# Kernel tuning notes

Measured on AMD Instinct MI355X. Metric: run time of the kernel, lower is better.

## Reference

```python
import jax, jax.numpy as jnp
import numpy as np

K = 10
BN_EPS = 1e-5


def _edgeconv(x, W, b, gamma, beta):
    """DGCNN EdgeConv: kNN on x, edge feat [x_i, x_j - x_i], Linear->(BN)->ReLU, max over k.
    x: [N, C]; W: [2C, Cout]; gamma/beta: [Cout] or None."""
    sq = jnp.sum(x * x, axis=1)                      # [N]
    dist = sq[:, None] + sq[None, :] - 2.0 * (x @ x.T)  # [N, N] squared dists
    _, idx = jax.lax.top_k(-dist, K)                 # [N, K] (includes self)
    xj = x[idx]                                      # [N, K, C] gather
    xi = jnp.broadcast_to(x[:, None, :], xj.shape)   # [N, K, C]
    e = jnp.concatenate([xi, xj - xi], axis=-1)      # [N, K, 2C]
    h = e @ W + b                                    # [N, K, Cout]
    if gamma is not None:                            # BatchNorm1d (training-mode batch stats)
        mu = h.mean(axis=(0, 1))
        var = h.var(axis=(0, 1))
        h = (h - mu) * jax.lax.rsqrt(var + BN_EPS) * gamma + beta
    h = jax.nn.relu(h)
    return h.max(axis=1)                             # [N, Cout]


def _aggregate(f, seg_ids, num_segments):
    return jax.ops.segment_max(f, seg_ids, num_segments=num_segments)


def setup_inputs() -> dict:
    key = jax.random.key(0)
    ks = jax.random.split(key, 12)
    N, B = 16384, 64
    x = jax.random.normal(ks[0], (N, 3), dtype=jnp.float32)
    n_pts = jnp.full((B,), N // B, dtype=jnp.int32)

    def lin(k, fi, fo):
        s = 1.0 / np.sqrt(fi)
        kw, kb = jax.random.split(k)
        return (jax.random.uniform(kw, (fi, fo), jnp.float32, -s, s),
                jax.random.uniform(kb, (fo,), jnp.float32, -s, s))

    W1, b1 = lin(ks[1], 6, 64)
    W2, b2 = lin(ks[2], 128, 64)
    W3, b3 = lin(ks[3], 128, 64)
    W4, b4 = lin(ks[4], 128, 64)
    Wp, bp = lin(ks[5], 256, 128)
    g1 = jnp.ones((64,), jnp.float32); be1 = jnp.zeros((64,), jnp.float32)
    g3 = jnp.ones((64,), jnp.float32); be3 = jnp.zeros((64,), jnp.float32)
    return {"x": x, "n_pts": n_pts,
            "W1": W1, "b1": b1, "g1": g1, "be1": be1,
            "W2": W2, "b2": b2,
            "W3": W3, "b3": b3, "g3": g3, "be3": be3,
            "W4": W4, "b4": b4,
            "Wp": Wp, "bp": bp}


def reference(x, n_pts, W1, b1, g1, be1, W2, b2, W3, b3, g3, be3, W4, b4, Wp, bp):
    N = x.shape[0]
    B = n_pts.shape[0]
    seg_ids = jnp.repeat(jnp.arange(B, dtype=jnp.int32), n_pts, total_repeat_length=N)

    f1 = _edgeconv(x,  W1, b1, g1,  be1)   # [N, 64]
    f2 = _edgeconv(f1, W2, b2, None, None)
    f3 = _edgeconv(f2, W3, b3, g3,  be3)
    f4 = _edgeconv(f3, W4, b4, None, None)

    p = jnp.concatenate([_aggregate(f, seg_ids, B) for f in (f1, f2, f3, f4)], axis=1)  # [B, 256]
    f = jnp.tanh(p @ Wp + bp)              # [B, 128]
    f = f / (jnp.linalg.norm(f, axis=1, keepdims=True) + 1e-9)
    return f
```

## Files before the change

### kernel.cpp

```cpp
#include <hip/hip_runtime.h>
#include <hip/hip_bf16.h>

constexpr int N = 16384;
constexpr int KNN = 10;
constexpr int CF = 64;
constexpr int NS64 = 12;
constexpr int NS3 = 12;

#define FBIG 1e30f

typedef __attribute__((ext_vector_type(8))) __bf16 bfv8;
typedef __attribute__((ext_vector_type(4))) float f32x4;

#define TOPK_INSERT(dval, jval)                                            \
  if ((dval) < bmax) {                                                     \
    float mv = bd[0]; int slot = 0;                                        \
    _Pragma("unroll") for (int s_ = 1; s_ < 10; ++s_)                      \
      if (bd[s_] > mv) { mv = bd[s_]; slot = s_; }                         \
    _Pragma("unroll") for (int s_ = 0; s_ < 10; ++s_)                      \
      if (slot == s_) { bd[s_] = (dval); bi[s_] = (jval); }                \
    bmax = bd[0];                                                          \
    _Pragma("unroll") for (int s_ = 1; s_ < 10; ++s_)                      \
      bmax = fmaxf(bmax, bd[s_]);                                          \
  }

__device__ inline ushort bf16_rne(float x) {
  unsigned u = __float_as_uint(x);
  return (ushort)((u + 0x7FFFu + ((u >> 16) & 1u)) >> 16);
}
__device__ inline float bf16_to_f(ushort h) { return __uint_as_float(((unsigned)h) << 16); }

__global__ __launch_bounds__(256) void pack3_kernel(const float* __restrict__ X,
                                                    float4* __restrict__ xp,
                                                    int* __restrict__ gtauI,
                                                    float* __restrict__ accum) {
  int i = blockIdx.x * 256 + threadIdx.x;
  float x0 = X[3 * i], x1 = X[3 * i + 1], x2 = X[3 * i + 2];
  float s = fmaf(x0, x0, fmaf(x1, x1, x2 * x2));
  xp[i] = make_float4(x0, x1, x2, s);
  gtauI[i] = 0x7F7F7F7F;
  if (blockIdx.x == 0 && threadIdx.x < 128) accum[threadIdx.x] = 0.f;
}

__global__ __launch_bounds__(256) void prep128s_kernel(const float* __restrict__ X,
                                                       ushort* __restrict__ Xp,
                                                       float* __restrict__ sq,
                                                       int* __restrict__ gtauI,
                                                       float* __restrict__ accum) {
  int i = blockIdx.x * 256 + threadIdx.x;
  int n = i >> 4, k4 = (i & 15) << 2;
  float4 v = ((const float4*)X)[i];
  float vv[4] = {v.x, v.y, v.z, v.w};
  ushort h[4], lo[4];
#pragma unroll
  for (int k = 0; k < 4; ++k) {
    h[k] = bf16_rne(vv[k]);
    lo[k] = bf16_rne(vv[k] - bf16_to_f(h[k]));
  }
  ushort* row = Xp + (size_t)n * 128;
  *(ushort4*)(row + k4) = make_ushort4(h[0], h[1], h[2], h[3]);
  *(ushort4*)(row + 64 + k4) = make_ushort4(lo[0], lo[1], lo[2], lo[3]);
  float ps = fmaf(vv[0], vv[0], fmaf(vv[1], vv[1], fmaf(vv[2], vv[2], vv[3] * vv[3])));
#pragma unroll
  for (int m = 1; m < 16; m <<= 1) ps += __shfl_xor(ps, m, 16);
  if ((threadIdx.x & 15) == 0) {
    sq[n] = ps;
    gtauI[n] = 0x7F7F7F7F;
  }
  if (blockIdx.x == 0 && threadIdx.x < 128) accum[threadIdx.x] = 0.f;
}

__global__ __launch_bounds__(256, 3) void knn64w_kernel(const ushort* __restrict__ Xp,
                                                        const float* __restrict__ sq,
                                                        int* __restrict__ gtauI,
                                                        float* __restrict__ dpart,
                                                        ushort* __restrict__ ipart) {
  __shared__ float bufD[4][64 * 33];
  __shared__ ushort bufI[4][64 * 34];
  __shared__ __align__(16) float tauS[4][64];
  __shared__ int cntS[4][64];

  const int tid = threadIdx.x;
  const int w = tid >> 6, l = tid & 63, lp = l & 15, g = l >> 4;
  const int rg = blockIdx.x / NS64, cs = blockIdx.x % NS64;
  const int wbase = rg * 256 + w * 64;
  const int myrow = wbase + l;
  const int c0 = (512 * cs) / NS64, c1 = (512 * (cs + 1)) / NS64;

  tauS[w][l] = FBIG;
  cntS[w][l] = 0;
  __builtin_amdgcn_wave_barrier();

  bfv8 aH1[4], aH2[4], aL1[4], aL2[4];
#pragma unroll
  for (int rt = 0; rt < 4; ++rt) {
    const size_t ao = (size_t)(wbase + rt * 16 + lp) * 128 + g * 8;
    aH1[rt] = *(const bfv8*)&Xp[ao];
    aH2[rt] = *(const bfv8*)&Xp[ao + 32];
    aL1[rt] = *(const bfv8*)&Xp[ao + 64];
    aL2[rt] = *(const bfv8*)&Xp[ao + 96];
  }
  float sqi[16];
#pragma unroll
  for (int rt = 0; rt < 4; ++rt)
#pragma unroll
    for (int r = 0; r < 4; ++r) sqi[rt * 4 + r] = sq[wbase + rt * 16 + g * 4 + r];

  float bd[10]; int bi[10]; float bmax = FBIG; float lastPub = FBIG;
#pragma unroll
  for (int s = 0; s < 10; ++s) { bd[s] = FBIG; bi[s] = 0x7fffffff; }
  int gt = 0x7F7F7F7F;

  for (int t = c0; t < c1; ++t) {
    const int col0 = t * 32 + lp;
    const int col1 = col0 + 16;
    const size_t bo0 = (size_t)col0 * 128 + g * 8;
    bfv8 p0 = *(const bfv8*)&Xp[bo0];
    bfv8 p1 = *(const bfv8*)&Xp[bo0 + 32];
    bfv8 p2 = *(const bfv8*)&Xp[bo0 + 64];
    bfv8 p3 = *(const bfv8*)&Xp[bo0 + 96];
    const size_t bo1 = (size_t)col1 * 128 + g * 8;
    bfv8 q0 = *(const bfv8*)&Xp[bo1];
    bfv8 q1 = *(const bfv8*)&Xp[bo1 + 32];
    bfv8 q2 = *(const bfv8*)&Xp[bo1 + 64];
    bfv8 q3 = *(const bfv8*)&Xp[bo1 + 96];
    float sj0 = sq[col0];
    float sj1 = sq[col1];
    int gtn = gtauI[myrow];

    __builtin_amdgcn_wave_barrier();
    {
      const int c = cntS[w][l];
      if (c) {
        const float* bD = &bufD[w][l * 33];
        const ushort* bI = &bufI[w][l * 34];
#pragma unroll 1
        for (int j = 0; j < c; ++j) {
          float d = bD[j];
          int ii = (int)bI[j];
          TOPK_INSERT(d, ii);
        }
        cntS[w][l] = 0;
      }
      tauS[w][l] = fminf(bmax, __int_as_float(gt));
      if (bmax < lastPub) {
        atomicMin(&gtauI[myrow], __float_as_int(bmax));
        lastPub = bmax;
      }
    }
    __builtin_amdgcn_wave_barrier();
    gt = gtn;

#pragma unroll
    for (int rt = 0; rt < 4; ++rt) {
      f32x4 taur = *(const f32x4*)&tauS[w][rt * 16 + g * 4];
      f32x4 acc0 = {0.f, 0.f, 0.f, 0.f};
      acc0 = __builtin_amdgcn_mfma_f32_16x16x32_bf16(aH1[rt], p0, acc0, 0, 0, 0);
      acc0 = __builtin_amdgcn_mfma_f32_16x16x32_bf16(aH2[rt], p1, acc0, 0, 0, 0);
      acc0 = __builtin_amdgcn_mfma_f32_16x16x32_bf16(aH1[rt], p2, acc0, 0, 0, 0);
      acc0 = __builtin_amdgcn_mfma_f32_16x16x32_bf16(aH2[rt], p3, acc0, 0, 0, 0);
      acc0 = __builtin_amdgcn_mfma_f32_16x16x32_bf16(aL1[rt], p0, acc0, 0, 0, 0);
      acc0 = __builtin_amdgcn_mfma_f32_16x16x32_bf16(aL2[rt], p1, acc0, 0, 0, 0);
      f32x4 acc1 = {0.f, 0.f, 0.f, 0.f};
      acc1 = __builtin_amdgcn_mfma_f32_16x16x32_bf16(aH1[rt], q0, acc1, 0, 0, 0);
      acc1 = __builtin_amdgcn_mfma_f32_16x16x32_bf16(aH2[rt], q1, acc1, 0, 0, 0);
      acc1 = __builtin_amdgcn_mfma_f32_16x16x32_bf16(aH1[rt], q2, acc1, 0, 0, 0);
      acc1 = __builtin_amdgcn_mfma_f32_16x16x32_bf16(aH2[rt], q3, acc1, 0, 0, 0);
      acc1 = __builtin_amdgcn_mfma_f32_16x16x32_bf16(aL1[rt], q0, acc1, 0, 0, 0);
      acc1 = __builtin_amdgcn_mfma_f32_16x16x32_bf16(aL2[rt], q1, acc1, 0, 0, 0);
#pragma unroll
      for (int r = 0; r < 4; ++r) {
        const int rloc = rt * 16 + g * 4 + r;
        float d0 = fmaf(-2.f, acc0[r], sqi[rt * 4 + r] + sj0);
        if (d0 < taur[r]) {
          int pos = atomicAdd(&cntS[w][rloc], 1);
          bufD[w][rloc * 33 + pos] = d0;
          bufI[w][rloc * 34 + pos] = (ushort)col0;
        }
        float d1 = fmaf(-2.f, acc1[r], sqi[rt * 4 + r] + sj1);
        if (d1 < taur[r]) {
          int pos = atomicAdd(&cntS[w][rloc], 1);
          bufD[w][rloc * 33 + pos] = d1;
          bufI[w][rloc * 34 + pos] = (ushort)col1;
        }
      }
    }
  }

  __builtin_amdgcn_wave_barrier();
  {
    const int c = cntS[w][l];
    const float* bD = &bufD[w][l * 33];
    const ushort* bI = &bufI[w][l * 34];
#pragma unroll 1
    for (int j = 0; j < c; ++j) {
      float d = bD[j];
      int ii = (int)bI[j];
      TOPK_INSERT(d, ii);
    }
  }
  float* dp = dpart + ((size_t)cs * N + myrow) * 10;
  ushort* ip = ipart + ((size_t)cs * N + myrow) * 10;
#pragma unroll
  for (int s = 0; s < 10; ++s) { dp[s] = bd[s]; ip[s] = (ushort)bi[s]; }
}

__global__ __launch_bounds__(256, 3) void knn3g_kernel(const float4* __restrict__ xp,
                                                       int* __restrict__ gtauI,
                                                       float* __restrict__ dpart,
                                                       ushort* __restrict__ ipart) {
  __shared__ float bufD[4][64 * 33];
  __shared__ ushort bufI[4][64 * 34];
  __shared__ __align__(16) float tauS[4][64];
  __shared__ int cntS[4][64];

  const int tid = threadIdx.x;
  const int w = tid >> 6, l = tid & 63, lp = l & 15, g = l >> 4;
  const int rg = blockIdx.x / NS3, cs = blockIdx.x % NS3;
  const int wbase = rg * 256 + w * 64;
  const int myrow = wbase + l;
  const int c0 = (512 * cs) / NS3, c1 = (512 * (cs + 1)) / NS3;

  tauS[w][l] = FBIG;
  cntS[w][l] = 0;
  __builtin_amdgcn_wave_barrier();

  float4 rw[16];
#pragma unroll
  for (int rt = 0; rt < 4; ++rt)
#pragma unroll
    for (int r = 0; r < 4; ++r) rw[rt * 4 + r] = xp[wbase + rt * 16 + g * 4 + r];

  float bd[10]; int bi[10]; float bmax = FBIG; float lastPub = FBIG;
#pragma unroll
  for (int s = 0; s < 10; ++s) { bd[s] = FBIG; bi[s] = 0x7fffffff; }
  int gt = 0x7F7F7F7F;

  for (int t = c0; t < c1; ++t) {
    const int col0 = t * 32 + lp;
    const int col1 = col0 + 16;
    const float4 oc0 = xp[col0];
    const float4 oc1 = xp[col1];
    int gtn = gtauI[myrow];

    __builtin_amdgcn_wave_barrier();
    {
      const int c = cntS[w][l];
      if (c) {
        const float* bD = &bufD[w][l * 33];
        const ushort* bI = &bufI[w][l * 34];
#pragma unroll 1
        for (int j = 0; j < c; ++j) {
          float d = bD[j];
          int ii = (int)bI[j];
          TOPK_INSERT(d, ii);
        }
        cntS[w][l] = 0;
      }
      tauS[w][l] = fminf(bmax, __int_as_float(gt));
      if (bmax < lastPub) {
        atomicMin(&gtauI[myrow], __float_as_int(bmax));
        lastPub = bmax;
      }
    }
    __builtin_amdgcn_wave_barrier();
    gt = gtn;

#pragma unroll
    for (int rt = 0; rt < 4; ++rt) {
      f32x4 taur = *(const f32x4*)&tauS[w][rt * 16 + g * 4];
#pragma unroll
      for (int r = 0; r < 4; ++r) {
        const float4 m = rw[rt * 4 + r];
        const int rloc = rt * 16 + g * 4 + r;
        float dot0 = fmaf(m.x, oc0.x, fmaf(m.y, oc0.y, m.z * oc0.z));
        float d0 = fmaf(-2.f, dot0, m.w + oc0.w);
        if (d0 < taur[r]) {
          int pos = atomicAdd(&cntS[w][rloc], 1);
          bufD[w][rloc * 33 + pos] = d0;
          bufI[w][rloc * 34 + pos] = (ushort)col0;
        }
        float dot1 = fmaf(m.x, oc1.x, fmaf(m.y, oc1.y, m.z * oc1.z));
        float d1 = fmaf(-2.f, dot1, m.w + oc1.w);
        if (d1 < taur[r]) {
          int pos = atomicAdd(&cntS[w][rloc], 1);
          bufD[w][rloc * 33 + pos] = d1;
          bufI[w][rloc * 34 + pos] = (ushort)col1;
        }
      }
    }
  }

  __builtin_amdgcn_wave_barrier();
  {
    const int c = cntS[w][l];
    const float* bD = &bufD[w][l * 33];
    const ushort* bI = &bufI[w][l * 34];
#pragma unroll 1
    for (int j = 0; j < c; ++j) {
      float d = bD[j];
      int ii = (int)bI[j];
      TOPK_INSERT(d, ii);
    }
  }
  float* dp = dpart + ((size_t)cs * N + myrow) * 10;
  ushort* ip = ipart + ((size_t)cs * N + myrow) * 10;
#pragma unroll
  for (int s = 0; s < 10; ++s) { dp[s] = bd[s]; ip[s] = (ushort)bi[s]; }
}

template <int S>
__global__ __launch_bounds__(256) void merge_kernel(const float* __restrict__ dpart,
                                                    const ushort* __restrict__ ipart,
                                                    ushort* __restrict__ idx_out) {
  const int row = blockIdx.x * 256 + threadIdx.x;
  float d[S * 10]; int id_[S * 10];
#pragma unroll
  for (int p = 0; p < S; ++p)
#pragma unroll
    for (int s = 0; s < 10; ++s) {
      d[p * 10 + s] = dpart[((size_t)p * N + row) * 10 + s];
      id_[p * 10 + s] = (int)ipart[((size_t)p * N + row) * 10 + s];
    }
#pragma unroll
  for (int t = 0; t < 10; ++t) {
    float dm = d[0]; int im = id_[0]; int slot = 0;
#pragma unroll
    for (int e = 1; e < S * 10; ++e) {
      bool better = (d[e] < dm) || (d[e] == dm && id_[e] < im);
      if (better) { dm = d[e]; im = id_[e]; slot = e; }
    }
    idx_out[(size_t)row * 10 + t] = (ushort)im;
#pragma unroll
    for (int e = 0; e < S * 10; ++e)
      if (e == slot) d[e] = FBIG;
  }
}

__global__ __launch_bounds__(256) void uv_kernel(const float* __restrict__ Xf, int CIN,
                                                 const float* __restrict__ W,
                                                 const float* __restrict__ bias,
                                                 float* __restrict__ U, float* __restrict__ V) {
  __shared__ float Ws[8192];
  int tid = threadIdx.x;
  int c = tid & 63, p = tid >> 6;
  int n = blockIdx.x * 4 + p;
  const int tot = CIN * 128;
  for (int i = tid; i < tot; i += 256) Ws[i] = W[i];
  __syncthreads();
  const float* xr = Xf + (size_t)n * CIN;
  float vt = 0.f, vb = 0.f;
  for (int m = 0; m < CIN; ++m) {
    float xm = xr[m];
    vt = fmaf(xm, Ws[m * 64 + c], vt);
    vb = fmaf(xm, Ws[(CIN + m) * 64 + c], vb);
  }
  U[(size_t)n * 64 + c] = vb;
  V[(size_t)n * 64 + c] = vt - vb + bias[c];
}

__global__ __launch_bounds__(256) void stats_kernel(const float* __restrict__ U,
                                                    const float* __restrict__ V,
                                                    const ushort* __restrict__ idx,
                                                    float* __restrict__ accum) {
  int tid = threadIdx.x;
  int c = tid & 63, p = tid >> 6;
  int base = blockIdx.x * 64;
  float s = 0.f, s2 = 0.f;
  for (int ch = 0; ch < 16; ++ch) {
    int n = base + ch * 4 + p;
    float vn = V[(size_t)n * 64 + c];
    const ushort* in_ = idx + (size_t)n * 10;
#pragma unroll
    for (int k = 0; k < 10; ++k) {
      float h = vn + U[(size_t)in_[k] * 64 + c];
      s += h;
      s2 = fmaf(h, h, s2);
    }
  }
  __shared__ float red[256], red2[256];
  red[tid] = s; red2[tid] = s2;
  __syncthreads();
  if (tid < 64) {
    float ts = red[tid] + red[64 + tid] + red[128 + tid] + red[192 + tid];
    float t2 = red2[tid] + red2[64 + tid] + red2[128 + tid] + red2[192 + tid];
    atomicAdd(&accum[tid], ts);
    atomicAdd(&accum[64 + tid], t2);
  }
}

__global__ void bnfin_kernel(const float* __restrict__ accum,
                             const float* __restrict__ gamma,
                             const float* __restrict__ beta,
                             float* __restrict__ scale, float* __restrict__ shift) {
  int c = threadIdx.x;
  float inv = 1.f / (float)(N * KNN);
  float mu = accum[c] * inv;
  float var = accum[64 + c] * inv - mu * mu;
  float sc = gamma[c] * rsqrtf(var + 1e-5f);
  scale[c] = sc;
  shift[c] = fmaf(-mu, sc, beta[c]);
}

__global__ __launch_bounds__(256) void apply_kernel(const float* __restrict__ U,
                                                    const float* __restrict__ V,
                                                    const ushort* __restrict__ idx,
                                                    const float* __restrict__ scale,
                                                    const float* __restrict__ shift,
                                                    int use_bn, float* __restrict__ Fout) {
  int tid = threadIdx.x;
  int c = tid & 63, p = tid >> 6;
  int n = blockIdx.x * 4 + p;
  float sc = use_bn ? scale[c] : 1.f;
  float sh = use_bn ? shift[c] : 0.f;
  float vn = V[(size_t)n * 64 + c];
  const ushort* in_ = idx + (size_t)n * 10;
  float m = 0.f;
#pragma unroll
  for (int k = 0; k < 10; ++k) {
    float h = vn + U[(size_t)in_[k] * 64 + c];
    m = fmaxf(m, fmaf(h, sc, sh));
  }
  Fout[(size_t)n * 64 + c] = m;
}

__global__ __launch_bounds__(256) void pool1_kernel(const float* __restrict__ f1,
                                                    const float* __restrict__ f2,
                                                    const float* __restrict__ f3,
                                                    const float* __restrict__ f4,
                                                    const int* __restrict__ n_pts,
                                                    float* __restrict__ Pp) {
  int b = blockIdx.x >> 2;
  int q = blockIdx.x & 3;
  int c = threadIdx.x;
  int off = 0;
  for (int i = 0; i < b; ++i) off += n_pts[i];
  int cnt_ = n_pts[b];
  int s0 = off + (cnt_ * q) / 4;
  int s1 = off + (cnt_ * (q + 1)) / 4;
  const float* f = (c < 64) ? f1 : (c < 128) ? f2 : (c < 192) ? f3 : f4;
  int ch = c & 63;
  float m = -3.4e38f;
  for (int t = s0; t < s1; ++t) m = fmaxf(m, f[(size_t)t * 64 + ch]);
  Pp[((size_t)q * 64 + b) * 256 + c] = m;
}

__global__ __launch_bounds__(128) void head_kernel(const float* __restrict__ Pp,
                                                   const float* __restrict__ Wp,
                                                   const float* __restrict__ bp,
                                                   float* __restrict__ out) {
  int b = blockIdx.x;
  int c = threadIdx.x;
  __shared__ float ps[256];
#pragma unroll
  for (int j = 0; j < 2; ++j) {
    int cc = c + j * 128;
    float m = Pp[(size_t)b * 256 + cc];
#pragma unroll
    for (int q = 1; q < 4; ++q) m = fmaxf(m, Pp[((size_t)q * 64 + b) * 256 + cc]);
    ps[cc] = m;
  }
  __syncthreads();
  float acc = bp[c];
  for (int m = 0; m < 256; ++m) acc = fmaf(ps[m], Wp[m * 128 + c], acc);
  float t = tanhf(acc);
  __shared__ float red[128];
  red[c] = t * t;
  __syncthreads();
  for (int s = 64; s > 0; s >>= 1) {
    if (c < s) red[c] += red[c + s];
    __syncthreads();
  }
  float nrm = sqrtf(red[0]);
  out[b * 128 + c] = t / (nrm + 1e-9f);
}

extern "C" void kernel_launch(void* const* d_in, const int* in_sizes, int n_in,
                              void* d_out, int out_size, void* d_ws, size_t ws_size,
                              hipStream_t stream) {
  const float* x = (const float*)d_in[0];
  const int* n_pts = (const int*)d_in[1];
  const float* W1 = (const float*)d_in[2];
  const float* b1 = (const float*)d_in[3];
  const float* g1 = (const float*)d_in[4];
  const float* be1 = (const float*)d_in[5];
  const float* W2 = (const float*)d_in[6];
  const float* b2 = (const float*)d_in[7];
  const float* W3 = (const float*)d_in[8];
  const float* b3 = (const float*)d_in[9];
  const float* g3 = (const float*)d_in[10];
  const float* be3 = (const float*)d_in[11];
  const float* W4 = (const float*)d_in[12];
  const float* b4 = (const float*)d_in[13];
  const float* Wp = (const float*)d_in[14];
  const float* bp = (const float*)d_in[15];
  float* out = (float*)d_out;

  char* w = (char*)d_ws;
  auto alloc = [&](size_t bytes) {
    char* p = w;
    w += (bytes + 255) & ~(size_t)255;
    return p;
  };
  const size_t FS = (size_t)N * 64 * 4;
  float* f1 = (float*)alloc(FS);
  float* f2 = (float*)alloc(FS);
  float* f3 = (float*)alloc(FS);
  float* f4 = (float*)alloc(FS);
  float* Ub = (float*)alloc(FS);
  float* dpartf = (float*)alloc((size_t)NS64 * N * 10 * 4);
  ushort* iparti = (ushort*)alloc((size_t)NS64 * N * 10 * 2);
  float4* xp = (float4*)alloc((size_t)N * 16);
  float* sqb = (float*)alloc((size_t)N * 4);
  int* gtauI = (int*)alloc((size_t)N * 4);
  ushort* idxb = (ushort*)alloc((size_t)N * 10 * 2);
  float* accum = (float*)alloc(512);
  float* scaleb = (float*)alloc(256);
  float* shiftb = (float*)alloc(256);
  float* Ppart = (float*)alloc((size_t)4 * 64 * 256 * 4);
  ushort* Xp128 = (ushort*)Ub;
  float* Vb = dpartf;
  (void)ws_size; (void)n_in; (void)in_sizes; (void)out_size;

  auto run_layer = [&](const float* fin, int cin, const float* W, const float* b,
                       const float* g, const float* be, int use_bn, float* fout) {
    if (cin == 3) {
      pack3_kernel<<<N / 256, 256, 0, stream>>>(fin, xp, gtauI, accum);
      knn3g_kernel<<<64 * NS3, 256, 0, stream>>>(xp, gtauI, dpartf, iparti);
      merge_kernel<NS3><<<N / 256, 256, 0, stream>>>(dpartf, iparti, idxb);
    } else {
      prep128s_kernel<<<N * 64 / 4 / 256, 256, 0, stream>>>(fin, Xp128, sqb, gtauI, accum);
      knn64w_kernel<<<64 * NS64, 256, 0, stream>>>(Xp128, sqb, gtauI, dpartf, iparti);
      merge_kernel<NS64><<<N / 256, 256, 0, stream>>>(dpartf, iparti, idxb);
    }
    uv_kernel<<<N / 4, 256, 0, stream>>>(fin, cin, W, b, Ub, Vb);
    if (use_bn) {
      stats_kernel<<<256, 256, 0, stream>>>(Ub, Vb, idxb, accum);
      bnfin_kernel<<<1, 64, 0, stream>>>(accum, g, be, scaleb, shiftb);
    }
    apply_kernel<<<N / 4, 256, 0, stream>>>(Ub, Vb, idxb, scaleb, shiftb, use_bn, fout);
  };

  run_layer(x, 3, W1, b1, g1, be1, 1, f1);
  run_layer(f1, 64, W2, b2, nullptr, nullptr, 0, f2);
  run_layer(f2, 64, W3, b3, g3, be3, 1, f3);
  run_layer(f3, 64, W4, b4, nullptr, nullptr, 0, f4);
  pool1_kernel<<<256, 256, 0, stream>>>(f1, f2, f3, f4, n_pts, Ppart);
  head_kernel<<<64, 128, 0, stream>>>(Ppart, Wp, bp, out);
}
```

Before: 1.222 ms.

## Fold squared-norm terms into extra MFMA via augmented bf16 row layout

Extends each packed row from 128 to 192 bf16 values, adding a block that encodes the squared norm (split into three bf16 parts) alongside constant ones. An extra MFMA per tile then yields sq_i + sq_j directly, and the A operands are pre-scaled by -2, so the distance comes straight out of the accumulator. This drops the per-element fma and the scalar sq loads in the kNN inner loop. In exchange it adds one more MFMA per accumulator, raises per-row load bandwidth by half, and slightly changes rounding of the distances.

```diff
diff --git a/kernel.cpp b/kernel.cpp
--- a/kernel.cpp
+++ b/kernel.cpp
@@ -30,6 +30,14 @@
 }
 __device__ inline float bf16_to_f(ushort h) { return __uint_as_float(((unsigned)h) << 16); }
 
+__device__ inline bfv8 scale_m2(bfv8 v) {
+  union { bfv8 b; ushort u[8]; } a, r;
+  a.b = v;
+#pragma unroll
+  for (int k = 0; k < 8; ++k) r.u[k] = bf16_rne(-2.f * bf16_to_f(a.u[k]));
+  return r.b;
+}
+
 __global__ __launch_bounds__(256) void pack3_kernel(const float* __restrict__ X,
                                                     float4* __restrict__ xp,
                                                     int* __restrict__ gtauI,
@@ -42,11 +50,10 @@
   if (blockIdx.x == 0 && threadIdx.x < 128) accum[threadIdx.x] = 0.f;
 }
 
-__global__ __launch_bounds__(256) void prep128s_kernel(const float* __restrict__ X,
-                                                       ushort* __restrict__ Xp,
-                                                       float* __restrict__ sq,
-                                                       int* __restrict__ gtauI,
-                                                       float* __restrict__ accum) {
+__global__ __launch_bounds__(256) void prep192_kernel(const float* __restrict__ X,
+                                                      ushort* __restrict__ Xp,
+                                                      int* __restrict__ gtauI,
+                                                      float* __restrict__ accum) {
   int i = blockIdx.x * 256 + threadIdx.x;
   int n = i >> 4, k4 = (i & 15) << 2;
   float4 v = ((const float4*)X)[i];
@@ -57,21 +64,30 @@
     h[k] = bf16_rne(vv[k]);
     lo[k] = bf16_rne(vv[k] - bf16_to_f(h[k]));
   }
-  ushort* row = Xp + (size_t)n * 128;
+  ushort* row = Xp + (size_t)n * 192;
   *(ushort4*)(row + k4) = make_ushort4(h[0], h[1], h[2], h[3]);
   *(ushort4*)(row + 64 + k4) = make_ushort4(lo[0], lo[1], lo[2], lo[3]);
   float ps = fmaf(vv[0], vv[0], fmaf(vv[1], vv[1], fmaf(vv[2], vv[2], vv[3] * vv[3])));
 #pragma unroll
   for (int m = 1; m < 16; m <<= 1) ps += __shfl_xor(ps, m, 16);
-  if ((threadIdx.x & 15) == 0) {
-    sq[n] = ps;
-    gtauI[n] = 0x7F7F7F7F;
-  }
+  ushort sh = bf16_rne(ps);
+  float r1 = ps - bf16_to_f(sh);
+  ushort sm = bf16_rne(r1);
+  float r2 = r1 - bf16_to_f(sm);
+  ushort sl = bf16_rne(r2);
+  const ushort one = 0x3F80;
+  int j = k4 >> 2;
+  ushort4 mw = make_ushort4(0, 0, 0, 0);
+  if (j == 0) mw = make_ushort4(one, one, one, sh);
+  else if (j == 1) mw = make_ushort4(sm, sl, 0, 0);
+  else if (j == 8) mw = make_ushort4(sh, sm, sl, one);
+  else if (j == 9) mw = make_ushort4(one, one, 0, 0);
+  *(ushort4*)(row + 128 + k4) = mw;
+  if ((i & 15) == 0) gtauI[n] = 0x7F7F7F7F;
   if (blockIdx.x == 0 && threadIdx.x < 128) accum[threadIdx.x] = 0.f;
 }
 
 __global__ __launch_bounds__(256, 3) void knn64w_kernel(const ushort* __restrict__ Xp,
-                                                        const float* __restrict__ sq,
                                                         int* __restrict__ gtauI,
                                                         float* __restrict__ dpart,
                                                         ushort* __restrict__ ipart) {
@@ -91,41 +107,38 @@
   cntS[w][l] = 0;
   __builtin_amdgcn_wave_barrier();
 
-  bfv8 aH1[4], aH2[4], aL1[4], aL2[4];
+  bfv8 aH1[4], aH2[4], aL1[4], aL2[4], aE[4];
 #pragma unroll
   for (int rt = 0; rt < 4; ++rt) {
-    const size_t ao = (size_t)(wbase + rt * 16 + lp) * 128 + g * 8;
-    aH1[rt] = *(const bfv8*)&Xp[ao];
-    aH2[rt] = *(const bfv8*)&Xp[ao + 32];
-    aL1[rt] = *(const bfv8*)&Xp[ao + 64];
-    aL2[rt] = *(const bfv8*)&Xp[ao + 96];
-  }
-  float sqi[16];
-#pragma unroll
-  for (int rt = 0; rt < 4; ++rt)
-#pragma unroll
-    for (int r = 0; r < 4; ++r) sqi[rt * 4 + r] = sq[wbase + rt * 16 + g * 4 + r];
+    const size_t ao = (size_t)(wbase + rt * 16 + lp) * 192 + g * 8;
+    aH1[rt] = scale_m2(*(const bfv8*)&Xp[ao]);
+    aH2[rt] = scale_m2(*(const bfv8*)&Xp[ao + 32]);
+    aL1[rt] = scale_m2(*(const bfv8*)&Xp[ao + 64]);
+    aL2[rt] = scale_m2(*(const bfv8*)&Xp[ao + 96]);
+    aE[rt] = *(const bfv8*)&Xp[ao + 160];
+  }
 
   float bd[10]; int bi[10]; float bmax = FBIG; float lastPub = FBIG;
 #pragma unroll
   for (int s = 0; s < 10; ++s) { bd[s] = FBIG; bi[s] = 0x7fffffff; }
   int gt = 0x7F7F7F7F;
+  const f32x4 z4 = {0.f, 0.f, 0.f, 0.f};
 
   for (int t = c0; t < c1; ++t) {
     const int col0 = t * 32 + lp;
     const int col1 = col0 + 16;
-    const size_t bo0 = (size_t)col0 * 128 + g * 8;
+    const size_t bo0 = (size_t)col0 * 192 + g * 8;
     bfv8 p0 = *(const bfv8*)&Xp[bo0];
     bfv8 p1 = *(const bfv8*)&Xp[bo0 + 32];
     bfv8 p2 = *(const bfv8*)&Xp[bo0 + 64];
     bfv8 p3 = *(const bfv8*)&Xp[bo0 + 96];
-    const size_t bo1 = (size_t)col1 * 128 + g * 8;
+    bfv8 pe0 = *(const bfv8*)&Xp[bo0 + 128];
+    const size_t bo1 = (size_t)col1 * 192 + g * 8;
     bfv8 q0 = *(const bfv8*)&Xp[bo1];
     bfv8 q1 = *(const bfv8*)&Xp[bo1 + 32];
     bfv8 q2 = *(const bfv8*)&Xp[bo1 + 64];
     bfv8 q3 = *(const bfv8*)&Xp[bo1 + 96];
-    float sj0 = sq[col0];
-    float sj1 = sq[col1];
+    bfv8 pe1 = *(const bfv8*)&Xp[bo1 + 128];
     int gtn = gtauI[myrow];
 
     __builtin_amdgcn_wave_barrier();
@@ -154,14 +167,14 @@
 #pragma unroll
     for (int rt = 0; rt < 4; ++rt) {
       f32x4 taur = *(const f32x4*)&tauS[w][rt * 16 + g * 4];
-      f32x4 acc0 = {0.f, 0.f, 0.f, 0.f};
+      f32x4 acc0 = __builtin_amdgcn_mfma_f32_16x16x32_bf16(aE[rt], pe0, z4, 0, 0, 0);
       acc0 = __builtin_amdgcn_mfma_f32_16x16x32_bf16(aH1[rt], p0, acc0, 0, 0, 0);
       acc0 = __builtin_amdgcn_mfma_f32_16x16x32_bf16(aH2[rt], p1, acc0, 0, 0, 0);
       acc0 = __builtin_amdgcn_mfma_f32_16x16x32_bf16(aH1[rt], p2, acc0, 0, 0, 0);
       acc0 = __builtin_amdgcn_mfma_f32_16x16x32_bf16(aH2[rt], p3, acc0, 0, 0, 0);
       acc0 = __builtin_amdgcn_mfma_f32_16x16x32_bf16(aL1[rt], p0, acc0, 0, 0, 0);
       acc0 = __builtin_amdgcn_mfma_f32_16x16x32_bf16(aL2[rt], p1, acc0, 0, 0, 0);
-      f32x4 acc1 = {0.f, 0.f, 0.f, 0.f};
+      f32x4 acc1 = __builtin_amdgcn_mfma_f32_16x16x32_bf16(aE[rt], pe1, z4, 0, 0, 0);
       acc1 = __builtin_amdgcn_mfma_f32_16x16x32_bf16(aH1[rt], q0, acc1, 0, 0, 0);
       acc1 = __builtin_amdgcn_mfma_f32_16x16x32_bf16(aH2[rt], q1, acc1, 0, 0, 0);
       acc1 = __builtin_amdgcn_mfma_f32_16x16x32_bf16(aH1[rt], q2, acc1, 0, 0, 0);
@@ -171,13 +184,13 @@
 #pragma unroll
       for (int r = 0; r < 4; ++r) {
         const int rloc = rt * 16 + g * 4 + r;
-        float d0 = fmaf(-2.f, acc0[r], sqi[rt * 4 + r] + sj0);
+        float d0 = acc0[r];
         if (d0 < taur[r]) {
           int pos = atomicAdd(&cntS[w][rloc], 1);
           bufD[w][rloc * 33 + pos] = d0;
           bufI[w][rloc * 34 + pos] = (ushort)col0;
         }
-        float d1 = fmaf(-2.f, acc1[r], sqi[rt * 4 + r] + sj1);
+        float d1 = acc1[r];
         if (d1 < taur[r]) {
           int pos = atomicAdd(&cntS[w][rloc], 1);
           bufD[w][rloc * 33 + pos] = d1;
@@ -510,15 +523,14 @@
   float* Ub = (float*)alloc(FS);
   float* dpartf = (float*)alloc((size_t)NS64 * N * 10 * 4);
   ushort* iparti = (ushort*)alloc((size_t)NS64 * N * 10 * 2);
+  ushort* Xp192 = (ushort*)alloc((size_t)N * 192 * 2);
   float4* xp = (float4*)alloc((size_t)N * 16);
-  float* sqb = (float*)alloc((size_t)N * 4);
   int* gtauI = (int*)alloc((size_t)N * 4);
   ushort* idxb = (ushort*)alloc((size_t)N * 10 * 2);
   float* accum = (float*)alloc(512);
   float* scaleb = (float*)alloc(256);
   float* shiftb = (float*)alloc(256);
   float* Ppart = (float*)alloc((size_t)4 * 64 * 256 * 4);
-  ushort* Xp128 = (ushort*)Ub;
   float* Vb = dpartf;
   (void)ws_size; (void)n_in; (void)in_sizes; (void)out_size;
 
@@ -529,8 +541,8 @@
       knn3g_kernel<<<64 * NS3, 256, 0, stream>>>(xp, gtauI, dpartf, iparti);
       merge_kernel<NS3><<<N / 256, 256, 0, stream>>>(dpartf, iparti, idxb);
     } else {
-      prep128s_kernel<<<N * 64 / 4 / 256, 256, 0, stream>>>(fin, Xp128, sqb, gtauI, accum);
-      knn64w_kernel<<<64 * NS64, 256, 0, stream>>>(Xp128, sqb, gtauI, dpartf, iparti);
+      prep192_kernel<<<N / 16, 256, 0, stream>>>(fin, Xp192, gtauI, accum);
+      knn64w_kernel<<<64 * NS64, 256, 0, stream>>>(Xp192, gtauI, dpartf, iparti);
       merge_kernel<NS64><<<N / 256, 256, 0, stream>>>(dpartf, iparti, idxb);
     }
     uv_kernel<<<N / 4, 256, 0, stream>>>(fin, cin, W, b, Ub, Vb);
```

Result: slower. 1.496 ms (+22.4%).

## Restructure kNN kernels: per-lane row top-k, drop LDS candidate buffers

Applied to the files above, without the earlier changes.

Redesigns the kNN kernels so each wave handles 16 rows, and each lane keeps a private top-10 for one row over a quarter of the columns. Candidates are inserted directly into registers instead of being staged in shared-memory buffers with atomics and wave barriers. Column splits drop from 12 to 4 per row while the grid grows, giving 16 partial lists per row. The merge kernel becomes a streaming top-10 insert instead of a full selection over all partials. The aim is to remove LDS atomic and barrier overhead and raise occupancy, at the cost of more divergent per-lane inserts and a larger merge input.

```diff
diff --git a/kernel.cpp b/kernel.cpp
--- a/kernel.cpp
+++ b/kernel.cpp
@@ -4,8 +4,8 @@
 constexpr int N = 16384;
 constexpr int KNN = 10;
 constexpr int CF = 64;
-constexpr int NS64 = 12;
-constexpr int NS3 = 12;
+constexpr int NS64 = 4;
+constexpr int NS3 = 4;
 
 #define FBIG 1e30f
 
@@ -70,41 +70,24 @@
   if (blockIdx.x == 0 && threadIdx.x < 128) accum[threadIdx.x] = 0.f;
 }
 
-__global__ __launch_bounds__(256, 3) void knn64w_kernel(const ushort* __restrict__ Xp,
+__global__ __launch_bounds__(256, 4) void knn64w_kernel(const ushort* __restrict__ Xp,
                                                         const float* __restrict__ sq,
                                                         int* __restrict__ gtauI,
                                                         float* __restrict__ dpart,
                                                         ushort* __restrict__ ipart) {
-  __shared__ float bufD[4][64 * 33];
-  __shared__ ushort bufI[4][64 * 34];
-  __shared__ __align__(16) float tauS[4][64];
-  __shared__ int cntS[4][64];
-
   const int tid = threadIdx.x;
   const int w = tid >> 6, l = tid & 63, lp = l & 15, g = l >> 4;
   const int rg = blockIdx.x / NS64, cs = blockIdx.x % NS64;
-  const int wbase = rg * 256 + w * 64;
-  const int myrow = wbase + l;
+  const int rowbase = rg * 64 + w * 16;
+  const int myrow = rowbase + lp;
   const int c0 = (512 * cs) / NS64, c1 = (512 * (cs + 1)) / NS64;
 
-  tauS[w][l] = FBIG;
-  cntS[w][l] = 0;
-  __builtin_amdgcn_wave_barrier();
-
-  bfv8 aH1[4], aH2[4], aL1[4], aL2[4];
-#pragma unroll
-  for (int rt = 0; rt < 4; ++rt) {
-    const size_t ao = (size_t)(wbase + rt * 16 + lp) * 128 + g * 8;
-    aH1[rt] = *(const bfv8*)&Xp[ao];
-    aH2[rt] = *(const bfv8*)&Xp[ao + 32];
-    aL1[rt] = *(const bfv8*)&Xp[ao + 64];
-    aL2[rt] = *(const bfv8*)&Xp[ao + 96];
-  }
-  float sqi[16];
-#pragma unroll
-  for (int rt = 0; rt < 4; ++rt)
-#pragma unroll
-    for (int r = 0; r < 4; ++r) sqi[rt * 4 + r] = sq[wbase + rt * 16 + g * 4 + r];
+  const size_t ro = (size_t)myrow * 128 + g * 8;
+  const bfv8 rH1 = *(const bfv8*)&Xp[ro];
+  const bfv8 rH2 = *(const bfv8*)&Xp[ro + 32];
+  const bfv8 rL1 = *(const bfv8*)&Xp[ro + 64];
+  const bfv8 rL2 = *(const bfv8*)&Xp[ro + 96];
+  const float sqrow = sq[myrow];
 
   float bd[10]; int bi[10]; float bmax = FBIG; float lastPub = FBIG;
 #pragma unroll
@@ -112,124 +95,75 @@
   int gt = 0x7F7F7F7F;
 
   for (int t = c0; t < c1; ++t) {
-    const int col0 = t * 32 + lp;
-    const int col1 = col0 + 16;
-    const size_t bo0 = (size_t)col0 * 128 + g * 8;
-    bfv8 p0 = *(const bfv8*)&Xp[bo0];
-    bfv8 p1 = *(const bfv8*)&Xp[bo0 + 32];
-    bfv8 p2 = *(const bfv8*)&Xp[bo0 + 64];
-    bfv8 p3 = *(const bfv8*)&Xp[bo0 + 96];
-    const size_t bo1 = (size_t)col1 * 128 + g * 8;
-    bfv8 q0 = *(const bfv8*)&Xp[bo1];
-    bfv8 q1 = *(const bfv8*)&Xp[bo1 + 32];
-    bfv8 q2 = *(const bfv8*)&Xp[bo1 + 64];
-    bfv8 q3 = *(const bfv8*)&Xp[bo1 + 96];
-    float sj0 = sq[col0];
-    float sj1 = sq[col1];
+    const size_t ao0 = (size_t)(t * 32 + lp) * 128 + g * 8;
+    const bfv8 c0H1 = *(const bfv8*)&Xp[ao0];
+    const bfv8 c0H2 = *(const bfv8*)&Xp[ao0 + 32];
+    const bfv8 c0L1 = *(const bfv8*)&Xp[ao0 + 64];
+    const bfv8 c0L2 = *(const bfv8*)&Xp[ao0 + 96];
+    const size_t ao1 = (size_t)(t * 32 + 16 + lp) * 128 + g * 8;
+    const bfv8 c1H1 = *(const bfv8*)&Xp[ao1];
+    const bfv8 c1H2 = *(const bfv8*)&Xp[ao1 + 32];
+    const bfv8 c1L1 = *(const bfv8*)&Xp[ao1 + 64];
+    const bfv8 c1L2 = *(const bfv8*)&Xp[ao1 + 96];
+    const f32x4 s4a = *(const f32x4*)&sq[t * 32 + g * 4];
+    const f32x4 s4b = *(const f32x4*)&sq[t * 32 + 16 + g * 4];
     int gtn = gtauI[myrow];
 
-    __builtin_amdgcn_wave_barrier();
-    {
-      const int c = cntS[w][l];
-      if (c) {
-        const float* bD = &bufD[w][l * 33];
-        const ushort* bI = &bufI[w][l * 34];
-#pragma unroll 1
-        for (int j = 0; j < c; ++j) {
-          float d = bD[j];
-          int ii = (int)bI[j];
-          TOPK_INSERT(d, ii);
-        }
-        cntS[w][l] = 0;
+    f32x4 acc0 = {0.f, 0.f, 0.f, 0.f};
+    acc0 = __builtin_amdgcn_mfma_f32_16x16x32_bf16(c0H1, rH1, acc0, 0, 0, 0);
+    acc0 = __builtin_amdgcn_mfma_f32_16x16x32_bf16(c0H2, rH2, acc0, 0, 0, 0);
+    acc0 = __builtin_amdgcn_mfma_f32_16x16x32_bf16(c0L1, rH1, acc0, 0, 0, 0);
+    acc0 = __builtin_amdgcn_mfma_f32_16x16x32_bf16(c0L2, rH2, acc0, 0, 0, 0);
+    acc0 = __builtin_amdgcn_mfma_f32_16x16x32_bf16(c0H1, rL1, acc0, 0, 0, 0);
+    acc0 = __builtin_amdgcn_mfma_f32_16x16x32_bf16(c0H2, rL2, acc0, 0, 0, 0);
+    f32x4 acc1 = {0.f, 0.f, 0.f, 0.f};
+    acc1 = __builtin_amdgcn_mfma_f32_16x16x32_bf16(c1H1, rH1, acc1, 0, 0, 0);
+    acc1 = __builtin_amdgcn_mfma_f32_16x16x32_bf16(c1H2, rH2, acc1, 0, 0, 0);
+    acc1 = __builtin_amdgcn_mfma_f32_16x16x32_bf16(c1L1, rH1, acc1, 0, 0, 0);
+    acc1 = __builtin_amdgcn_mfma_f32_16x16x32_bf16(c1L2, rH2, acc1, 0, 0, 0);
+    acc1 = __builtin_amdgcn_mfma_f32_16x16x32_bf16(c1H1, rL1, acc1, 0, 0, 0);
+    acc1 = __builtin_amdgcn_mfma_f32_16x16x32_bf16(c1H2, rL2, acc1, 0, 0, 0);
+
+    const float gtf = __int_as_float(gt);
+#pragma unroll
+    for (int r = 0; r < 4; ++r) {
+      float d0 = fmaf(-2.f, acc0[r], sqrow + s4a[r]);
+      if (d0 < fminf(bmax, gtf)) {
+        int jj = t * 32 + g * 4 + r;
+        TOPK_INSERT(d0, jj)
       }
-      tauS[w][l] = fminf(bmax, __int_as_float(gt));
-      if (bmax < lastPub) {
-        atomicMin(&gtauI[myrow], __float_as_int(bmax));
-        lastPub = bmax;
+      float d1 = fmaf(-2.f, acc1[r], sqrow + s4b[r]);
+      if (d1 < fminf(bmax, gtf)) {
+        int jj = t * 32 + 16 + g * 4 + r;
+        TOPK_INSERT(d1, jj)
       }
     }
-    __builtin_amdgcn_wave_barrier();
     gt = gtn;
-
-#pragma unroll
-    for (int rt = 0; rt < 4; ++rt) {
-      f32x4 taur = *(const f32x4*)&tauS[w][rt * 16 + g * 4];
-      f32x4 acc0 = {0.f, 0.f, 0.f, 0.f};
-      acc0 = __builtin_amdgcn_mfma_f32_16x16x32_bf16(aH1[rt], p0, acc0, 0, 0, 0);
-      acc0 = __builtin_amdgcn_mfma_f32_16x16x32_bf16(aH2[rt], p1, acc0, 0, 0, 0);
-      acc0 = __builtin_amdgcn_mfma_f32_16x16x32_bf16(aH1[rt], p2, acc0, 0, 0, 0);
-      acc0 = __builtin_amdgcn_mfma_f32_16x16x32_bf16(aH2[rt], p3, acc0, 0, 0, 0);
-      acc0 = __builtin_amdgcn_mfma_f32_16x16x32_bf16(aL1[rt], p0, acc0, 0, 0, 0);
-      acc0 = __builtin_amdgcn_mfma_f32_16x16x32_bf16(aL2[rt], p1, acc0, 0, 0, 0);
-      f32x4 acc1 = {0.f, 0.f, 0.f, 0.f};
-      acc1 = __builtin_amdgcn_mfma_f32_16x16x32_bf16(aH1[rt], q0, acc1, 0, 0, 0);
-      acc1 = __builtin_amdgcn_mfma_f32_16x16x32_bf16(aH2[rt], q1, acc1, 0, 0, 0);
-      acc1 = __builtin_amdgcn_mfma_f32_16x16x32_bf16(aH1[rt], q2, acc1, 0, 0, 0);
-      acc1 = __builtin_amdgcn_mfma_f32_16x16x32_bf16(aH2[rt], q3, acc1, 0, 0, 0);
-      acc1 = __builtin_amdgcn_mfma_f32_16x16x32_bf16(aL1[rt], q0, acc1, 0, 0, 0);
-      acc1 = __builtin_amdgcn_mfma_f32_16x16x32_bf16(aL2[rt], q1, acc1, 0, 0, 0);
-#pragma unroll
-      for (int r = 0; r < 4; ++r) {
-        const int rloc = rt * 16 + g * 4 + r;
-        float d0 = fmaf(-2.f, acc0[r], sqi[rt * 4 + r] + sj0);
-        if (d0 < taur[r]) {
-          int pos = atomicAdd(&cntS[w][rloc], 1);
-          bufD[w][rloc * 33 + pos] = d0;
-          bufI[w][rloc * 34 + pos] = (ushort)col0;
-        }
-        float d1 = fmaf(-2.f, acc1[r], sqi[rt * 4 + r] + sj1);
-        if (d1 < taur[r]) {
-          int pos = atomicAdd(&cntS[w][rloc], 1);
-          bufD[w][rloc * 33 + pos] = d1;
-          bufI[w][rloc * 34 + pos] = (ushort)col1;
-        }
-      }
-    }
-  }
-
-  __builtin_amdgcn_wave_barrier();
-  {
-    const int c = cntS[w][l];
-    const float* bD = &bufD[w][l * 33];
-    const ushort* bI = &bufI[w][l * 34];
-#pragma unroll 1
-    for (int j = 0; j < c; ++j) {
-      float d = bD[j];
-      int ii = (int)bI[j];
-      TOPK_INSERT(d, ii);
-    }
-  }
-  float* dp = dpart + ((size_t)cs * N + myrow) * 10;
-  ushort* ip = ipart + ((size_t)cs * N + myrow) * 10;
+    if (bmax < lastPub) {
+      atomicMin(&gtauI[myrow], __float_as_int(bmax));
+      lastPub = bmax;
+    }
+  }
+
+  float* dp = dpart + ((size_t)(cs * 4 + g) * N + myrow) * 10;
+  ushort* ip = ipart + ((size_t)(cs * 4 + g) * N + myrow) * 10;
 #pragma unroll
   for (int s = 0; s < 10; ++s) { dp[s] = bd[s]; ip[s] = (ushort)bi[s]; }
 }
 
-__global__ __launch_bounds__(256, 3) void knn3g_kernel(const float4* __restrict__ xp,
+__global__ __launch_bounds__(256, 4) void knn3g_kernel(const float4* __restrict__ xp,
                                                        int* __restrict__ gtauI,
                                                        float* __restrict__ dpart,
                                                        ushort* __restrict__ ipart) {
-  __shared__ float bufD[4][64 * 33];
-  __shared__ ushort bufI[4][64 * 34];
-  __shared__ __align__(16) float tauS[4][64];
-  __shared__ int cntS[4][64];
-
   const int tid = threadIdx.x;
   const int w = tid >> 6, l = tid & 63, lp = l & 15, g = l >> 4;
   const int rg = blockIdx.x / NS3, cs = blockIdx.x % NS3;
-  const int wbase = rg * 256 + w * 64;
-  const int myrow = wbase + l;
+  const int rowbase = rg * 64 + w * 16;
+  const int myrow = rowbase + lp;
   const int c0 = (512 * cs) / NS3, c1 = (512 * (cs + 1)) / NS3;
 
-  tauS[w][l] = FBIG;
-  cntS[w][l] = 0;
-  __builtin_amdgcn_wave_barrier();
-
-  float4 rw[16];
-#pragma unroll
-  for (int rt = 0; rt < 4; ++rt)
-#pragma unroll
-    for (int r = 0; r < 4; ++r) rw[rt * 4 + r] = xp[wbase + rt * 16 + g * 4 + r];
+  const float4 m = xp[myrow];
+  const float sqrow = m.w;
 
   float bd[10]; int bi[10]; float bmax = FBIG; float lastPub = FBIG;
 #pragma unroll
@@ -237,74 +171,38 @@
   int gt = 0x7F7F7F7F;
 
   for (int t = c0; t < c1; ++t) {
-    const int col0 = t * 32 + lp;
-    const int col1 = col0 + 16;
-    const float4 oc0 = xp[col0];
-    const float4 oc1 = xp[col1];
+    float4 ca[4], cb[4];
+#pragma unroll
+    for (int r = 0; r < 4; ++r) {
+      ca[r] = xp[t * 32 + g * 4 + r];
+      cb[r] = xp[t * 32 + 16 + g * 4 + r];
+    }
     int gtn = gtauI[myrow];
-
-    __builtin_amdgcn_wave_barrier();
-    {
-      const int c = cntS[w][l];
-      if (c) {
-        const float* bD = &bufD[w][l * 33];
-        const ushort* bI = &bufI[w][l * 34];
-#pragma unroll 1
-        for (int j = 0; j < c; ++j) {
-          float d = bD[j];
-          int ii = (int)bI[j];
-          TOPK_INSERT(d, ii);
-        }
-        cntS[w][l] = 0;
+    const float gtf = __int_as_float(gt);
+#pragma unroll
+    for (int r = 0; r < 4; ++r) {
+      float dot0 = fmaf(m.x, ca[r].x, fmaf(m.y, ca[r].y, m.z * ca[r].z));
+      float d0 = fmaf(-2.f, dot0, sqrow + ca[r].w);
+      if (d0 < fminf(bmax, gtf)) {
+        int jj = t * 32 + g * 4 + r;
+        TOPK_INSERT(d0, jj)
       }
-      tauS[w][l] = fminf(bmax, __int_as_float(gt));
-      if (bmax < lastPub) {
-        atomicMin(&gtauI[myrow], __float_as_int(bmax));
-        lastPub = bmax;
+      float dot1 = fmaf(m.x, cb[r].x, fmaf(m.y, cb[r].y, m.z * cb[r].z));
+      float d1 = fmaf(-2.f, dot1, sqrow + cb[r].w);
+      if (d1 < fminf(bmax, gtf)) {
+        int jj = t * 32 + 16 + g * 4 + r;
+        TOPK_INSERT(d1, jj)
       }
     }
-    __builtin_amdgcn_wave_barrier();
     gt = gtn;
-
-#pragma unroll
-    for (int rt = 0; rt < 4; ++rt) {
-      f32x4 taur = *(const f32x4*)&tauS[w][rt * 16 + g * 4];
-#pragma unroll
-      for (int r = 0; r < 4; ++r) {
-        const float4 m = rw[rt * 4 + r];
-        const int rloc = rt * 16 + g * 4 + r;
-        float dot0 = fmaf(m.x, oc0.x, fmaf(m.y, oc0.y, m.z * oc0.z));
-        float d0 = fmaf(-2.f, dot0, m.w + oc0.w);
-        if (d0 < taur[r]) {
-          int pos = atomicAdd(&cntS[w][rloc], 1);
-          bufD[w][rloc * 33 + pos] = d0;
-          bufI[w][rloc * 34 + pos] = (ushort)col0;
-        }
-        float dot1 = fmaf(m.x, oc1.x, fmaf(m.y, oc1.y, m.z * oc1.z));
-        float d1 = fmaf(-2.f, dot1, m.w + oc1.w);
-        if (d1 < taur[r]) {
-          int pos = atomicAdd(&cntS[w][rloc], 1);
-          bufD[w][rloc * 33 + pos] = d1;
-          bufI[w][rloc * 34 + pos] = (ushort)col1;
-        }
-      }
-    }
-  }
-
-  __builtin_amdgcn_wave_barrier();
-  {
-    const int c = cntS[w][l];
-    const float* bD = &bufD[w][l * 33];
-    const ushort* bI = &bufI[w][l * 34];
-#pragma unroll 1
-    for (int j = 0; j < c; ++j) {
-      float d = bD[j];
-      int ii = (int)bI[j];
-      TOPK_INSERT(d, ii);
-    }
-  }
-  float* dp = dpart + ((size_t)cs * N + myrow) * 10;
-  ushort* ip = ipart + ((size_t)cs * N + myrow) * 10;
+    if (bmax < lastPub) {
+      atomicMin(&gtauI[myrow], __float_as_int(bmax));
+      lastPub = bmax;
+    }
+  }
+
+  float* dp = dpart + ((size_t)(cs * 4 + g) * N + myrow) * 10;
+  ushort* ip = ipart + ((size_t)(cs * 4 + g) * N + myrow) * 10;
 #pragma unroll
   for (int s = 0; s < 10; ++s) { dp[s] = bd[s]; ip[s] = (ushort)bi[s]; }
 }
@@ -314,27 +212,38 @@
                                                     const ushort* __restrict__ ipart,
                                                     ushort* __restrict__ idx_out) {
   const int row = blockIdx.x * 256 + threadIdx.x;
-  float d[S * 10]; int id_[S * 10];
-#pragma unroll
-  for (int p = 0; p < S; ++p)
+  float bd[10]; int bi[10];
+#pragma unroll
+  for (int s = 0; s < 10; ++s) { bd[s] = FBIG; bi[s] = 0x7fffffff; }
+  float bmax = FBIG; int bmaxi = 0x7fffffff;
+#pragma unroll 1
+  for (int p = 0; p < S; ++p) {
+    const float* dp = dpart + ((size_t)p * N + row) * 10;
+    const ushort* ip = ipart + ((size_t)p * N + row) * 10;
 #pragma unroll
     for (int s = 0; s < 10; ++s) {
-      d[p * 10 + s] = dpart[((size_t)p * N + row) * 10 + s];
-      id_[p * 10 + s] = (int)ipart[((size_t)p * N + row) * 10 + s];
-    }
-#pragma unroll
-  for (int t = 0; t < 10; ++t) {
-    float dm = d[0]; int im = id_[0]; int slot = 0;
-#pragma unroll
-    for (int e = 1; e < S * 10; ++e) {
-      bool better = (d[e] < dm) || (d[e] == dm && id_[e] < im);
-      if (better) { dm = d[e]; im = id_[e]; slot = e; }
-    }
-    idx_out[(size_t)row * 10 + t] = (ushort)im;
-#pragma unroll
-    for (int e = 0; e < S * 10; ++e)
-      if (e == slot) d[e] = FBIG;
-  }
+      float d = dp[s]; int ii = (int)ip[s];
+      if (d < bmax || (d == bmax && ii < bmaxi)) {
+        int slot = 0; float mv = bd[0]; int mi = bi[0];
+#pragma unroll
+        for (int e = 1; e < 10; ++e) {
+          bool gtr = (bd[e] > mv) || (bd[e] == mv && bi[e] > mi);
+          if (gtr) { mv = bd[e]; mi = bi[e]; slot = e; }
+        }
+#pragma unroll
+        for (int e = 0; e < 10; ++e)
+          if (e == slot) { bd[e] = d; bi[e] = ii; }
+        bmax = bd[0]; bmaxi = bi[0];
+#pragma unroll
+        for (int e = 1; e < 10; ++e) {
+          bool gtr = (bd[e] > bmax) || (bd[e] == bmax && bi[e] > bmaxi);
+          if (gtr) { bmax = bd[e]; bmaxi = bi[e]; }
+        }
+      }
+    }
+  }
+#pragma unroll
+  for (int t = 0; t < 10; ++t) idx_out[(size_t)row * 10 + t] = (ushort)bi[t];
 }
 
 __global__ __launch_bounds__(256) void uv_kernel(const float* __restrict__ Xf, int CIN,
@@ -503,13 +412,14 @@
     return p;
   };
   const size_t FS = (size_t)N * 64 * 4;
+  const int NPART = NS64 * 4;
   float* f1 = (float*)alloc(FS);
   float* f2 = (float*)alloc(FS);
   float* f3 = (float*)alloc(FS);
   float* f4 = (float*)alloc(FS);
   float* Ub = (float*)alloc(FS);
-  float* dpartf = (float*)alloc((size_t)NS64 * N * 10 * 4);
-  ushort* iparti = (ushort*)alloc((size_t)NS64 * N * 10 * 2);
+  float* dpartf = (float*)alloc((size_t)NPART * N * 10 * 4);
+  ushort* iparti = (ushort*)alloc((size_t)NPART * N * 10 * 2);
   float4* xp = (float4*)alloc((size_t)N * 16);
   float* sqb = (float*)alloc((size_t)N * 4);
   int* gtauI = (int*)alloc((size_t)N * 4);
@@ -526,12 +436,12 @@
                        const float* g, const float* be, int use_bn, float* fout) {
     if (cin == 3) {
       pack3_kernel<<<N / 256, 256, 0, stream>>>(fin, xp, gtauI, accum);
-      knn3g_kernel<<<64 * NS3, 256, 0, stream>>>(xp, gtauI, dpartf, iparti);
-      merge_kernel<NS3><<<N / 256, 256, 0, stream>>>(dpartf, iparti, idxb);
+      knn3g_kernel<<<(N / 64) * NS3, 256, 0, stream>>>(xp, gtauI, dpartf, iparti);
+      merge_kernel<16><<<N / 256, 256, 0, stream>>>(dpartf, iparti, idxb);
     } else {
       prep128s_kernel<<<N * 64 / 4 / 256, 256, 0, stream>>>(fin, Xp128, sqb, gtauI, accum);
-      knn64w_kernel<<<64 * NS64, 256, 0, stream>>>(Xp128, sqb, gtauI, dpartf, iparti);
-      merge_kernel<NS64><<<N / 256, 256, 0, stream>>>(dpartf, iparti, idxb);
+      knn64w_kernel<<<(N / 64) * NS64, 256, 0, stream>>>(Xp128, sqb, gtauI, dpartf, iparti);
+      merge_kernel<16><<<N / 256, 256, 0, stream>>>(dpartf, iparti, idxb);
     }
     uv_kernel<<<N / 4, 256, 0, stream>>>(fin, cin, W, b, Ub, Vb);
     if (use_bn) {
```

After: 3.382 ms. +176.7%, slower.
